# Kernel tuning notes

Measured on AMD Instinct MI355X. Metric: run time of the kernel, lower is better.

Reference implementation:

```python
import jax, jax.numpy as jnp
import numpy as np

TARGET_FIDELITY = 0.95
WEIGHT = 0.1
BATCH, DIM = 8192, 2048


def setup_inputs() -> dict:
    key = jax.random.key(0)
    k1, k2 = jax.random.split(key)
    # Scale by 1/sqrt(DIM) so each row is roughly unit-norm (quantum-state-like)
    # and the trace fidelity lands strictly inside the clamp interval [0, 1].
    scale = 1.0 / np.sqrt(DIM)
    latent_codes = jax.random.normal(k1, (BATCH, DIM), dtype=jnp.float32) * scale
    target_codes = jax.random.normal(k2, (BATCH, DIM), dtype=jnp.float32) * scale
    return {"latent_codes": latent_codes, "target_codes": target_codes}


def reference(latent_codes, target_codes):
    batch = latent_codes.shape[0]
    # rho = mean_i z_i z_i^T  ==  L^T L / B  (single GEMM instead of B outer products)
    rho = jnp.matmul(latent_codes.T, latent_codes) / batch      # [D, D]
    sigma = jnp.matmul(target_codes.T, target_codes) / batch    # [D, D]
    # trace(rho @ sigma) = sum(rho * sigma) since both are symmetric
    fidelity = jnp.clip(jnp.sum(rho * sigma), 0.0, 1.0)
    loss = WEIGHT * jnp.abs(fidelity - TARGET_FIDELITY)
    return loss
```

## Files before the change

### kernel.cpp

```cpp
#include <hip/hip_runtime.h>
#include <stdint.h>

#define BATCH 8192
#define DIM   2048
#define NT    272
#define QTOT  (NT * 32)
#define QPB   17
#define NSLOT 768

typedef unsigned char  u8;
typedef unsigned short u16;
typedef unsigned int   u32;

using v8i   = __attribute__((ext_vector_type(8)))  int;
using v16f  = __attribute__((ext_vector_type(16))) float;
using f32x4 = __attribute__((ext_vector_type(4)))  float;

#if __has_builtin(__builtin_amdgcn_cvt_scalef32_pk_fp4_f32)
#define HW_FP4 1
#endif

__device__ __forceinline__ void gl_lds16(const void* g, void* l) {
  __builtin_amdgcn_global_load_lds(
      (const __attribute__((address_space(1))) u32*)g,
      (__attribute__((address_space(3))) u32*)l, 16, 0, 0);
}

__device__ __forceinline__ int piece_base(int b) {
  const int m = b & 31;
  const int p = (m <= 16) ? (m >> 1) : (8 + ((m - 15) >> 1));
  return b + 16 * (b >> 5) + p;
}

__device__ __forceinline__ u32 nib4(float x) {
  float xs = x * 64.0f;
  float a  = fabsf(xs);
  u32 n = (u32)(a >= 0.25f) + (u32)(a >= 0.75f) + (u32)(a >= 1.25f) +
          (u32)(a >= 1.75f) + (u32)(a >= 2.5f)  + (u32)(a >= 3.5f)  +
          (u32)(a >= 5.0f);
  return n | (xs < 0.0f ? 8u : 0u);
}

__device__ __forceinline__ u16 pack4_fp4(float a, float b, float c, float d) {
#ifdef HW_FP4
  u32 w = __builtin_amdgcn_cvt_scalef32_pk_fp4_f32(0u,  a * 64.0f, b * 64.0f, 1.0f, 0);
  w     = __builtin_amdgcn_cvt_scalef32_pk_fp4_f32(w,   c * 64.0f, d * 64.0f, 1.0f, 1);
  return (u16)w;
#else
  return (u16)(nib4(a) | (nib4(b) << 4) | (nib4(c) << 8) | (nib4(d) << 12));
#endif
}

__global__ __launch_bounds__(256) void tcvt_fp4(
    const float* __restrict__ L, const float* __restrict__ T,
    u8* __restrict__ X, u8* __restrict__ Y,
    float* __restrict__ acc, u32* __restrict__ cnt)
{
  __shared__ u8 lsm[2][32768];

  const int tid = threadIdx.x;
  if (blockIdx.x == 0 && tid == 0) { *acc = 0.0f; *cnt = 0u; }

  int id = blockIdx.x;
  const float* src;
  u8* dst;
  if (id < 256) { src = L; dst = X; }
  else          { src = T; dst = Y; id -= 256; }
  const int d0 = (id & 7) * 256;
  const int b0 = (id >> 3) * 256;

  u32 outw[32];

#define STAGE(p, buf)                                                     \
  {                                                                       \
    const float* sp = src + (size_t)(b0 + (p) * 32) * DIM + d0;           \
    _Pragma("unroll")                                                     \
    for (int r = 0; r < 8; ++r) {                                         \
      const int li = r * 256 + tid;                                       \
      gl_lds16(sp + (size_t)(li >> 6) * DIM + (li & 63) * 4,              \
               &lsm[buf][li * 16]);                                       \
    }                                                                     \
  }

  STAGE(0, 0)

#pragma unroll
  for (int p = 0; p < 8; ++p) {
    __syncthreads();
    if (p < 7) STAGE(p + 1, (p + 1) & 1)
    const float* fb = (const float*)lsm[p & 1];
#pragma unroll
    for (int q = 0; q < 8; ++q) {
      const u16 w = pack4_fp4(fb[(4 * q + 0) * 256 + tid],
                              fb[(4 * q + 1) * 256 + tid],
                              fb[(4 * q + 2) * 256 + tid],
                              fb[(4 * q + 3) * 256 + tid]);
      const int Q = p * 8 + q;
      if (Q & 1) outw[Q >> 1] |= (u32)w << 16;
      else       outw[Q >> 1] = w;
    }
  }

  {
    u8* db = lsm[0];
#pragma unroll
    for (int c = 0; c < 8; ++c) {
      u32* d4 = (u32*)(db + c * 4096 + (tid >> 3) * 128 + ((tid & 7) ^ c) * 16);
      d4[0] = outw[c * 4 + 0]; d4[1] = outw[c * 4 + 1];
      d4[2] = outw[c * 4 + 2]; d4[3] = outw[c * 4 + 3];
    }
  }
  __syncthreads();

#pragma unroll
  for (int g = 0; g < 8; ++g) {
    const int dl = g * 32 + (tid >> 3);
    const int c  = tid & 7;
    const u8* sb = lsm[0] + c * 4096 + (dl >> 3) * 128 + ((dl & 7) ^ c) * 16;
    uint4 v = *(const uint4*)sb;
    *(uint4*)(dst + (size_t)(d0 + dl) * (BATCH / 2) + (b0 >> 1) + c * 16) = v;
  }
#undef STAGE
}

__global__ __launch_bounds__(256, 2) void gram_fp4(
    const u8* __restrict__ X, const u8* __restrict__ Y,
    float* __restrict__ P)
{
  __shared__ u8 ls[2][2][16384];

  const int tid = threadIdx.x;
  const int bid = blockIdx.x;

  const int wave = tid >> 6;
  const int lane = tid & 63;
  const int wr = (wave >> 1) * 64;
  const int wc = (wave & 1) * 64;
  const int lr = lane & 31;
  const int kh = lane >> 5;

  u32 sdst[4]; int srow[4], sgc16[4];
#pragma unroll
  for (int rr = 0; rr < 4; ++rr) {
    const int li  = rr * 256 + tid;
    const int row = li >> 3;
    const int p   = li & 7;
    sdst[rr]  = (u32)(row * 128 + p * 16);
    srow[rr]  = row;
    sgc16[rr] = (p ^ (row & 7)) * 16;
  }

  u32 fa[2][4], fb[2][4];
#pragma unroll
  for (int h = 0; h < 2; ++h) {
    const int ra = wr + h * 32 + lr;
    const int rb = wc + h * 32 + lr;
#pragma unroll
    for (int ks = 0; ks < 4; ++ks) {
      const int c = 2 * ks + kh;
      fa[h][ks] = (u32)(ra * 128 + (c ^ (ra & 7)) * 16);
      fb[h][ks] = (u32)(rb * 128 + (c ^ (rb & 7)) * 16);
    }
  }

  v16f acc[2][2] = {};
  const int sc = 0x7F7F7F7F;

  const int q0  = bid * QPB;
  const int t0b = q0 >> 5;
  const int sl0 = piece_base(bid);
  int cur_t = -1, buf = 0;
  bool diag = false;
  const u8* src = X;
  u32 soi[4], soj[4];

  for (int it = 0; it < QPB; ++it) {
    const int q = q0 + it;
    const int t = q >> 5;
    const int k = q & 31;

    if (t != cur_t) {
      const int ltile = (t < 136) ? t : t - 136;
      src = (t < 136) ? X : Y;
      int ti = 0;
      while ((ti + 1) * (ti + 2) / 2 <= ltile) ++ti;
      const int tj = ltile - ti * (ti + 1) / 2;
      const int i0 = ti * 128;
      const int j0 = tj * 128;
      diag = (ti == tj);
#pragma unroll
      for (int rr = 0; rr < 4; ++rr) {
        soi[rr] = (u32)(i0 + srow[rr]) * (BATCH / 2) + sgc16[rr];
        soj[rr] = (u32)(j0 + srow[rr]) * (BATCH / 2) + sgc16[rr];
      }
      const u32 kb = (u32)k * 128;
#pragma unroll
      for (int rr = 0; rr < 4; ++rr)
        gl_lds16(src + soi[rr] + kb, &ls[buf][0][sdst[rr]]);
      if (!diag)
#pragma unroll
        for (int rr = 0; rr < 4; ++rr)
          gl_lds16(src + soj[rr] + kb, &ls[buf][1][sdst[rr]]);
      if (cur_t >= 0) {
        float4* o = (float4*)(P + (size_t)(sl0 + (cur_t - t0b)) * 16384);
#pragma unroll
        for (int h = 0; h < 2; ++h)
#pragma unroll
          for (int hc = 0; hc < 2; ++hc)
#pragma unroll
            for (int r4 = 0; r4 < 4; ++r4) {
              float4 v = {acc[h][hc][r4 * 4 + 0], acc[h][hc][r4 * 4 + 1],
                          acc[h][hc][r4 * 4 + 2], acc[h][hc][r4 * 4 + 3]};
              o[((h * 2 + hc) * 4 + r4) * 256 + tid] = v;
            }
#pragma unroll
        for (int h = 0; h < 2; ++h)
#pragma unroll
          for (int hc = 0; hc < 2; ++hc)
#pragma unroll
            for (int c2 = 0; c2 < 16; ++c2)
              acc[h][hc][c2] = 0.0f;
      }
      cur_t = t;
    }

    __syncthreads();
    if (it + 1 < QPB && ((q + 1) >> 5) == t) {
      const u32 kb = (u32)(k + 1) * 128;
#pragma unroll
      for (int rr = 0; rr < 4; ++rr)
        gl_lds16(src + soi[rr] + kb, &ls[buf ^ 1][0][sdst[rr]]);
      if (!diag)
#pragma unroll
        for (int rr = 0; rr < 4; ++rr)
          gl_lds16(src + soj[rr] + kb, &ls[buf ^ 1][1][sdst[rr]]);
    }

    const u8* pI = ls[buf][0];
    const u8* pJ = diag ? ls[buf][0] : ls[buf][1];
#pragma unroll
    for (int ks = 0; ks < 4; ++ks) {
      v8i a[2], b[2];
#pragma unroll
      for (int h = 0; h < 2; ++h) {
        int4 pa = *(const int4*)&pI[fa[h][ks]];
        a[h] = (v8i){pa.x, pa.y, pa.z, pa.w, 0, 0, 0, 0};
        int4 pb = *(const int4*)&pJ[fb[h][ks]];
        b[h] = (v8i){pb.x, pb.y, pb.z, pb.w, 0, 0, 0, 0};
      }
#pragma unroll
      for (int h = 0; h < 2; ++h)
#pragma unroll
        for (int hc = 0; hc < 2; ++hc)
          acc[h][hc] = __builtin_amdgcn_mfma_scale_f32_32x32x64_f8f6f4(
              a[h], b[hc], acc[h][hc],  4,  4,
              0, sc, 0, sc);
    }
    buf ^= 1;
  }

  {
    float4* o = (float4*)(P + (size_t)(sl0 + (cur_t - t0b)) * 16384);
#pragma unroll
    for (int h = 0; h < 2; ++h)
#pragma unroll
      for (int hc = 0; hc < 2; ++hc)
#pragma unroll
        for (int r4 = 0; r4 < 4; ++r4) {
          float4 v = {acc[h][hc][r4 * 4 + 0], acc[h][hc][r4 * 4 + 1],
                      acc[h][hc][r4 * 4 + 2], acc[h][hc][r4 * 4 + 3]};
          o[((h * 2 + hc) * 4 + r4) * 256 + tid] = v;
        }
  }
}

__device__ __forceinline__ int collect_pieces(int t, int* s) {
  const int qlo = 32 * t, qhi = 32 * t + 31;
  const int b_lo = qlo / 17, b_hi = qhi / 17;
  int n = 0;
  for (int b = b_lo; b <= b_hi; ++b) {
    const int tfirst = (17 * b) >> 5;
    s[n++] = piece_base(b) + (t - tfirst);
  }
  return n;
}

__global__ __launch_bounds__(256) void dot_kernel(
    const float4* __restrict__ P4,
    float* __restrict__ d_acc, u32* __restrict__ d_cnt,
    float* __restrict__ out)
{
  __shared__ float red[4];
  const int tid  = threadIdx.x;
  const int lane = tid & 63;
  const int lt   = blockIdx.x >> 1;
  const int half = blockIdx.x & 1;

  int ti = 0;
  while ((ti + 1) * (ti + 2) / 2 <= lt) ++ti;
  const int tj = lt - ti * (ti + 1) / 2;
  const float w = (ti == tj) ? 1.0f : 2.0f;

  int sx[3], sy[3];
  const int nx = collect_pieces(lt, sx);
  const int ny = collect_pieces(136 + lt, sy);

  const size_t ho = (size_t)half * 2048;
  float s = 0.0f;
#pragma unroll
  for (int j = 0; j < 8; ++j) {
    const int e = tid + j * 256;
    float4 a = P4[(size_t)sx[0] * 4096 + ho + e];
    {
      float4 u = P4[(size_t)sx[1] * 4096 + ho + e];
      a.x += u.x; a.y += u.y; a.z += u.z; a.w += u.w;
    }
    if (nx == 3) {
      float4 u = P4[(size_t)sx[2] * 4096 + ho + e];
      a.x += u.x; a.y += u.y; a.z += u.z; a.w += u.w;
    }
    float4 b = P4[(size_t)sy[0] * 4096 + ho + e];
    {
      float4 u = P4[(size_t)sy[1] * 4096 + ho + e];
      b.x += u.x; b.y += u.y; b.z += u.z; b.w += u.w;
    }
    if (ny == 3) {
      float4 u = P4[(size_t)sy[2] * 4096 + ho + e];
      b.x += u.x; b.y += u.y; b.z += u.z; b.w += u.w;
    }
    s += a.x * b.x + a.y * b.y + a.z * b.z + a.w * b.w;
  }
  s *= w;
#pragma unroll
  for (int off = 32; off > 0; off >>= 1)
    s += __shfl_down(s, off);
  if (lane == 0) red[tid >> 6] = s;
  __syncthreads();
  if (tid == 0) {
    atomicAdd(d_acc, red[0] + red[1] + red[2] + red[3]);
    __threadfence();
    const u32 old = atomicAdd(d_cnt, 1u);
    if (old == 271u) {
      float S   = atomicAdd(d_acc, 0.0f);
      float fid = S * 0x1.0p-50f;
      fid = fminf(fmaxf(fid, 0.0f), 1.0f);
      *out = 0.1f * fabsf(fid - 0.95f);
    }
  }
}

extern "C" void kernel_launch(void* const* d_in, const int* in_sizes, int n_in,
                              void* d_out, int out_size, void* d_ws, size_t ws_size,
                              hipStream_t stream) {
  const float* L = (const float*)d_in[0];
  const float* T = (const float*)d_in[1];
  float* out = (float*)d_out;

  const size_t NF4 = (size_t)BATCH * DIM / 2;
  u8*    X   = (u8*)d_ws;
  u8*    Y   = (u8*)d_ws + NF4;
  float* P   = (float*)((char*)d_ws + 2 * NF4);
  float* acc = P + (size_t)NSLOT * 16384;
  u32*   cnt = (u32*)(acc + 1);

  tcvt_fp4<<<512, 256, 0, stream>>>(L, T, X, Y, acc, cnt);
  gram_fp4<<<512, 256, 0, stream>>>(X, Y, P);
  dot_kernel<<<272, 256, 0, stream>>>((const float4*)P, acc, cnt, out);
}
```

Baseline: 201.1 us.

## Restructure FP4 transpose-convert to full-row tiles and drop LDS transpose stage

The conversion kernel now gives each block 32 full batch rows across all 2048 columns, loaded as contiguous 32 KB chunks, with 512 threads per block. Each thread owns four columns, packs their values across the 32 rows into 16 bytes, and writes them directly to the transposed FP4 output. This removes the LDS swizzle and write-back stage along with one barrier. In exchange, each output store is a 16-byte piece strided by 4 KB between threads, so writes are less coalesced than before.

```diff
diff --git a/kernel.cpp b/kernel.cpp
--- a/kernel.cpp
+++ b/kernel.cpp
@@ -14,7 +14,6 @@
 
 using v8i   = __attribute__((ext_vector_type(8)))  int;
 using v16f  = __attribute__((ext_vector_type(16))) float;
-using f32x4 = __attribute__((ext_vector_type(4)))  float;
 
 #if __has_builtin(__builtin_amdgcn_cvt_scalef32_pk_fp4_f32)
 #define HW_FP4 1
@@ -51,7 +50,7 @@
 #endif
 }
 
-__global__ __launch_bounds__(256) void tcvt_fp4(
+__global__ __launch_bounds__(512) void tcvt_fp4(
     const float* __restrict__ L, const float* __restrict__ T,
     u8* __restrict__ X, u8* __restrict__ Y,
     float* __restrict__ acc, u32* __restrict__ cnt)
@@ -61,24 +60,23 @@
   const int tid = threadIdx.x;
   if (blockIdx.x == 0 && tid == 0) { *acc = 0.0f; *cnt = 0u; }
 
-  int id = blockIdx.x;
+  const int id = blockIdx.x;
   const float* src;
   u8* dst;
   if (id < 256) { src = L; dst = X; }
-  else          { src = T; dst = Y; id -= 256; }
-  const int d0 = (id & 7) * 256;
-  const int b0 = (id >> 3) * 256;
-
-  u32 outw[32];
+  else          { src = T; dst = Y; }
+  const int rg = id & 255;
+  const int b0 = rg * 32;
+
+  u32 outw[4][4];
 
 #define STAGE(p, buf)                                                     \
   {                                                                       \
-    const float* sp = src + (size_t)(b0 + (p) * 32) * DIM + d0;           \
+    const u8* sp = (const u8*)src + ((size_t)(b0 + (p) * 4) << 13);       \
     _Pragma("unroll")                                                     \
-    for (int r = 0; r < 8; ++r) {                                         \
-      const int li = r * 256 + tid;                                       \
-      gl_lds16(sp + (size_t)(li >> 6) * DIM + (li & 63) * 4,              \
-               &lsm[buf][li * 16]);                                       \
+    for (int r = 0; r < 4; ++r) {                                         \
+      const int li = r * 512 + tid;                                       \
+      gl_lds16(sp + (size_t)li * 16, &lsm[buf][li * 16]);                 \
     }                                                                     \
   }
 
@@ -90,37 +88,22 @@
     if (p < 7) STAGE(p + 1, (p + 1) & 1)
     const float* fb = (const float*)lsm[p & 1];
 #pragma unroll
-    for (int q = 0; q < 8; ++q) {
-      const u16 w = pack4_fp4(fb[(4 * q + 0) * 256 + tid],
-                              fb[(4 * q + 1) * 256 + tid],
-                              fb[(4 * q + 2) * 256 + tid],
-                              fb[(4 * q + 3) * 256 + tid]);
-      const int Q = p * 8 + q;
-      if (Q & 1) outw[Q >> 1] |= (u32)w << 16;
-      else       outw[Q >> 1] = w;
-    }
-  }
-
-  {
-    u8* db = lsm[0];
-#pragma unroll
-    for (int c = 0; c < 8; ++c) {
-      u32* d4 = (u32*)(db + c * 4096 + (tid >> 3) * 128 + ((tid & 7) ^ c) * 16);
-      d4[0] = outw[c * 4 + 0]; d4[1] = outw[c * 4 + 1];
-      d4[2] = outw[c * 4 + 2]; d4[3] = outw[c * 4 + 3];
-    }
-  }
-  __syncthreads();
-
-#pragma unroll
-  for (int g = 0; g < 8; ++g) {
-    const int dl = g * 32 + (tid >> 3);
-    const int c  = tid & 7;
-    const u8* sb = lsm[0] + c * 4096 + (dl >> 3) * 128 + ((dl & 7) ^ c) * 16;
-    uint4 v = *(const uint4*)sb;
-    *(uint4*)(dst + (size_t)(d0 + dl) * (BATCH / 2) + (b0 >> 1) + c * 16) = v;
+    for (int k = 0; k < 4; ++k) {
+      const int col = tid + k * 512;
+      const u16 w = pack4_fp4(fb[0 * 2048 + col], fb[1 * 2048 + col],
+                              fb[2 * 2048 + col], fb[3 * 2048 + col]);
+      if (p & 1) outw[k][p >> 1] |= (u32)w << 16;
+      else       outw[k][p >> 1]  = w;
+    }
   }
 #undef STAGE
+
+#pragma unroll
+  for (int k = 0; k < 4; ++k) {
+    const int d = tid + k * 512;
+    uint4 v = {outw[k][0], outw[k][1], outw[k][2], outw[k][3]};
+    *(uint4*)(dst + ((size_t)d << 12) + rg * 16) = v;
+  }
 }
 
 __global__ __launch_bounds__(256, 2) void gram_fp4(
@@ -363,7 +346,7 @@
   float* acc = P + (size_t)NSLOT * 16384;
   u32*   cnt = (u32*)(acc + 1);
 
-  tcvt_fp4<<<512, 256, 0, stream>>>(L, T, X, Y, acc, cnt);
+  tcvt_fp4<<<512, 512, 0, stream>>>(L, T, X, Y, acc, cnt);
   gram_fp4<<<512, 256, 0, stream>>>(X, Y, P);
   dot_kernel<<<272, 256, 0, stream>>>((const float4*)P, acc, cnt, out);
 }
```

Result: slower. 212.8 us (+5.8%).
